# Kernel optimization log

Hardware: AMD Instinct MI355X
Metric: run time of the kernel (lower is better)

Reference implementation:

```python
import jax, jax.numpy as jnp
import numpy as np

M = 262144      # total tokens
K = 64          # n_channels (input dim)
N = 64          # expert_size (output dim)
E = 8           # n_experts


def setup_inputs() -> dict:
    key = jax.random.key(0)
    k1, k2, k3 = jax.random.split(key, 3)
    x = jax.random.normal(k1, (M, K), dtype=jnp.float32)
    sel = jax.random.randint(k2, (M,), 0, E, dtype=jnp.int32)
    w = jax.random.normal(k3, (E, K, N), dtype=jnp.float32)
    return {"x": x, "sel": sel, "w": w}


def reference(x, sel, w):
    # cvmm: out[m] = x[m] @ w[sel[m]]  (per-token expert GEMM)
    # Loop over the small fixed expert set; accumulate masked dense GEMMs
    # instead of materializing w[sel] ([M,K,N], which would be huge).
    E_ = w.shape[0]
    out = jnp.zeros((x.shape[0], w.shape[2]), dtype=x.dtype)
    for e in range(E_):
        mask = (sel == e)[:, None]           # [M,1]
        out = out + jnp.where(mask, x @ w[e], jnp.zeros((), x.dtype))
    return out
```

## Files before the change

kernel.cpp:

```cpp
#include <hip/hip_runtime.h>


typedef __bf16 bf16x8 __attribute__((ext_vector_type(8)));
typedef __bf16 bf16x4 __attribute__((ext_vector_type(4)));
typedef float  floatx4 __attribute__((ext_vector_type(4)));

#define CT 128

__global__ __launch_bounds__(256) void wpack_kernel(
    const float* __restrict__ w, bf16x8* __restrict__ wp)
{
    const int id   = blockIdx.x * 256 + threadIdx.x;
    const int lane = id & 63;
    const int nt   = (id >> 6) & 3;
    const int t    = (id >> 8) & 1;
    const int e    = id >> 9;
    const int q = lane >> 4, l16 = lane & 15;
    const float* src = w + (((e * 64) + t * 32 + q * 8) * 64) + nt * 16 + l16;
    bf16x8 f;
#pragma unroll
    for (int j = 0; j < 8; ++j) f[j] = (__bf16)src[j * 64];
    wp[id] = f;
}

__global__ __launch_bounds__(256, 3) void cvmm_kernel(
    const float* __restrict__ x,
    const int* __restrict__ sel,
    const bf16x8* __restrict__ wp,
    float* __restrict__ out)
{
    __shared__ __align__(16) unsigned char xls[CT * 128];
    __shared__ __align__(16) unsigned char obuf[CT * 272];
    __shared__ unsigned int sortLds[CT];
    __shared__ unsigned int invLds[CT];

    const int T    = threadIdx.x;
    const int lane = T & 63;
    const int wv   = T >> 6;
    const int q    = lane >> 4;
    const int l16  = lane & 15;

    const long tok0 = (long)blockIdx.x * CT;

    int s0 = 0, s1 = 0;
    if (wv == 0) {
        s0 = sel[tok0 + lane];
        s1 = sel[tok0 + 64 + lane];
    }

    const float* xb = x + tok0 * 64;
    floatx4 R[8];
#pragma unroll
    for (int i = 0; i < 8; ++i)
        R[i] = *(const floatx4*)(xb + i * 1024 + 4 * T);

    const bf16x8* wpw = wp + wv * 64 + lane;
    floatx4 bfp[8][2];
#pragma unroll
    for (int e = 0; e < 8; ++e) {
#pragma unroll
        for (int t = 0; t < 2; ++t)
            bfp[e][t] = __builtin_bit_cast(floatx4, wpw[e * 512 + t * 256]);
    }
#pragma unroll
    for (int e = 0; e < 8; ++e) {
        asm volatile("" : "+v"(bfp[e][0]), "+v"(bfp[e][1]));
    }

    if (wv == 0) {
        const unsigned long long lt = (1ull << lane) - 1;
        int slot0 = 0, slot1 = 0, pref = 0;
#pragma unroll
        for (int e = 0; e < 8; ++e) {
            unsigned long long m0 = __ballot(s0 == e);
            unsigned long long m1 = __ballot(s1 == e);
            if (s0 == e) slot0 = pref + __popcll(m0 & lt);
            if (s1 == e) slot1 = pref + __popcll(m0) + __popcll(m1 & lt);
            pref += __popcll(m0) + __popcll(m1);
        }
        invLds[lane]      = (unsigned)slot0;
        invLds[64 + lane] = (unsigned)slot1;
        sortLds[slot0] = (unsigned)lane        | ((unsigned)s0 << 8);
        sortLds[slot1] = (unsigned)(64 + lane) | ((unsigned)s1 << 8);
    }
    __syncthreads();

    {
        const int wrow = T >> 4;
        const int gl   = (T & 15) >> 1;
        const int half = (T & 1) * 8;
#pragma unroll
        for (int i = 0; i < 8; ++i) {
            const int slot = (int)invLds[i * 16 + wrow];
            bf16x4 v;
            v[0] = (__bf16)R[i][0]; v[1] = (__bf16)R[i][1];
            v[2] = (__bf16)R[i][2]; v[3] = (__bf16)R[i][3];
            *(bf16x4*)(xls + slot * 128 + ((gl ^ (slot & 7)) << 4) + half) = v;
        }
    }
    __syncthreads();

    {
        const int roffA = ((q)     ^ (l16 & 7)) << 4;
        const int roffB = ((q + 4) ^ (l16 & 7)) << 4;
        bf16x8 zf;
#pragma unroll
        for (int j = 0; j < 8; ++j) zf[j] = (__bf16)0.0f;

#pragma unroll
        for (int i = 0; i < 8; ++i) {
            const unsigned u = sortLds[i * 16 + l16];
            const int tokL = (int)(u & 255u);
            const int el   = (int)(u >> 8);
            const int rb   = (i * 16 + l16) * 128;
            const bf16x8 af0 = *(const bf16x8*)(xls + rb + roffA);
            const bf16x8 af1 = *(const bf16x8*)(xls + rb + roffB);
            const int elo = __builtin_amdgcn_readfirstlane(el);
            const int ehi = __builtin_amdgcn_readlane(el, 15);

            floatx4 acc = {0.0f, 0.0f, 0.0f, 0.0f};
#pragma unroll
            for (int e = 0; e < 8; ++e) {
                if (e >= elo && e <= ehi) {
                    const bool ok = (el == e);
                    acc = __builtin_amdgcn_mfma_f32_16x16x32_bf16(
                              __builtin_bit_cast(bf16x8, bfp[e][0]),
                              ok ? af0 : zf, acc, 0, 0, 0);
                    acc = __builtin_amdgcn_mfma_f32_16x16x32_bf16(
                              __builtin_bit_cast(bf16x8, bfp[e][1]),
                              ok ? af1 : zf, acc, 0, 0, 0);
                }
            }
            *(floatx4*)(obuf + tokL * 272 + (wv * 4 + q) * 16) = acc;
        }
    }
    __syncthreads();

    {
        float* og = out + tok0 * 64;
#pragma unroll
        for (int i = 0; i < 8; ++i) {
            const int G = i * 256 + T;
            const floatx4 v = *(const floatx4*)(obuf + (G >> 4) * 272 + (G & 15) * 16);
            *(floatx4*)(og + G * 4) = v;
        }
    }
}

extern "C" void kernel_launch(void* const* d_in, const int* in_sizes, int n_in,
                              void* d_out, int out_size, void* d_ws, size_t ws_size,
                              hipStream_t stream) {
    const float* x   = (const float*)d_in[0];
    const int*   sel = (const int*)d_in[1];
    const float* w   = (const float*)d_in[2];
    float*       out = (float*)d_out;

    const int M = in_sizes[0] / 64;
    bf16x8* wp = (bf16x8*)d_ws;

    wpack_kernel<<<16, 256, 0, stream>>>(w, wp);
    cvmm_kernel<<<M / CT, 256, 0, stream>>>(x, sel, wp, out);
}
```

Baseline: 121.4 us.

## Gather sorted x rows directly into LDS and fold weight packing into main kernel

Removes the separate weight-pack kernel: each block now loads and converts its fp32 weights to bf16 itself. The x tile is gathered in expert-sorted order straight into LDS as fp32 using global_load_lds, replacing the register staging and the inverse-permutation scatter. The output staging buffer reuses the x LDS region with an XOR swizzle, which frees LDS and raises the occupancy hint to 4 blocks per CU. The cost is redundant per-block weight reads and bf16 conversion, plus a larger fp32 x tile in LDS.

```diff
diff --git a/kernel.cpp b/kernel.cpp
--- a/kernel.cpp
+++ b/kernel.cpp
@@ -2,72 +2,43 @@
 
 
 typedef __bf16 bf16x8 __attribute__((ext_vector_type(8)));
-typedef __bf16 bf16x4 __attribute__((ext_vector_type(4)));
 typedef float  floatx4 __attribute__((ext_vector_type(4)));
 
 #define CT 128
 
-__global__ __launch_bounds__(256) void wpack_kernel(
-    const float* __restrict__ w, bf16x8* __restrict__ wp)
-{
-    const int id   = blockIdx.x * 256 + threadIdx.x;
-    const int lane = id & 63;
-    const int nt   = (id >> 6) & 3;
-    const int t    = (id >> 8) & 1;
-    const int e    = id >> 9;
-    const int q = lane >> 4, l16 = lane & 15;
-    const float* src = w + (((e * 64) + t * 32 + q * 8) * 64) + nt * 16 + l16;
-    bf16x8 f;
-#pragma unroll
-    for (int j = 0; j < 8; ++j) f[j] = (__bf16)src[j * 64];
-    wp[id] = f;
-}
+#define GLOAD_LDS16(g, l)                                        \
+    __builtin_amdgcn_global_load_lds(                            \
+        (const __attribute__((address_space(1))) void*)(g),      \
+        (__attribute__((address_space(3))) void*)(l), 16, 0, 0)
 
-__global__ __launch_bounds__(256, 3) void cvmm_kernel(
+#define BARL() do {                                        \
+    __builtin_amdgcn_sched_barrier(0);                     \
+    asm volatile("s_waitcnt lgkmcnt(0)" ::: "memory");     \
+    __builtin_amdgcn_s_barrier();                          \
+    __builtin_amdgcn_sched_barrier(0);                     \
+} while (0)
+
+__global__ __launch_bounds__(256, 4) void cvmm_kernel(
     const float* __restrict__ x,
     const int* __restrict__ sel,
-    const bf16x8* __restrict__ wp,
+    const float* __restrict__ w,
     float* __restrict__ out)
 {
-    __shared__ __align__(16) unsigned char xls[CT * 128];
-    __shared__ __align__(16) unsigned char obuf[CT * 272];
+    __shared__ __align__(16) unsigned char xls[CT * 256];
     __shared__ unsigned int sortLds[CT];
-    __shared__ unsigned int invLds[CT];
 
     const int T    = threadIdx.x;
     const int lane = T & 63;
     const int wv   = T >> 6;
     const int q    = lane >> 4;
     const int l16  = lane & 15;
+    const int n0   = wv << 4;
 
     const long tok0 = (long)blockIdx.x * CT;
 
-    int s0 = 0, s1 = 0;
     if (wv == 0) {
-        s0 = sel[tok0 + lane];
-        s1 = sel[tok0 + 64 + lane];
-    }
-
-    const float* xb = x + tok0 * 64;
-    floatx4 R[8];
-#pragma unroll
-    for (int i = 0; i < 8; ++i)
-        R[i] = *(const floatx4*)(xb + i * 1024 + 4 * T);
-
-    const bf16x8* wpw = wp + wv * 64 + lane;
-    floatx4 bfp[8][2];
-#pragma unroll
-    for (int e = 0; e < 8; ++e) {
-#pragma unroll
-        for (int t = 0; t < 2; ++t)
-            bfp[e][t] = __builtin_bit_cast(floatx4, wpw[e * 512 + t * 256]);
-    }
-#pragma unroll
-    for (int e = 0; e < 8; ++e) {
-        asm volatile("" : "+v"(bfp[e][0]), "+v"(bfp[e][1]));
-    }
-
-    if (wv == 0) {
+        const int s0 = sel[tok0 + lane];
+        const int s1 = sel[tok0 + 64 + lane];
         const unsigned long long lt = (1ull << lane) - 1;
         int slot0 = 0, slot1 = 0, pref = 0;
 #pragma unroll
@@ -78,71 +49,111 @@
             if (s1 == e) slot1 = pref + __popcll(m0) + __popcll(m1 & lt);
             pref += __popcll(m0) + __popcll(m1);
         }
-        invLds[lane]      = (unsigned)slot0;
-        invLds[64 + lane] = (unsigned)slot1;
         sortLds[slot0] = (unsigned)lane        | ((unsigned)s0 << 8);
         sortLds[slot1] = (unsigned)(64 + lane) | ((unsigned)s1 << 8);
     }
+
+    floatx4 bfp[8][2];
+#pragma unroll
+    for (int e = 0; e < 8; ++e)
+#pragma unroll
+        for (int t = 0; t < 2; ++t) {
+            const float* ws = w + ((e * 64 + t * 32 + q * 8) * 64) + (n0 + l16);
+            bf16x8 f;
+#pragma unroll
+            for (int j = 0; j < 8; ++j) f[j] = (__bf16)ws[j * 64];
+            bfp[e][t] = __builtin_bit_cast(floatx4, f);
+        }
+
+    BARL();
+
+    int tokA[8];
+#pragma unroll
+    for (int i = 0; i < 8; ++i) {
+        const int r    = i * 16 + wv * 4 + (lane >> 4);
+        const int tokR = (int)(sortLds[r] & 255u);
+        const int p    = (lane & 15) >> 1;
+        const int c    = p ^ (r & 7);
+        const float* g = x + (tok0 + tokR) * 64 + c * 8 + (lane & 1) * 4;
+        GLOAD_LDS16(g, xls + i * 4096 + wv * 1024);
+    }
+
+#pragma unroll
+    for (int i = 0; i < 8; ++i)
+        tokA[i] = (int)sortLds[i * 16 + l16];
+
+#pragma unroll
+    for (int e = 0; e < 8; ++e)
+        asm volatile("" : "+v"(bfp[e][0]), "+v"(bfp[e][1]));
+
     __syncthreads();
 
+    bf16x8 zf;
+#pragma unroll
+    for (int j = 0; j < 8; ++j) zf[j] = (__bf16)0.0f;
+
+    floatx4 acc[8];
+#pragma unroll
+    for (int i = 0; i < 8; ++i) {
+        const int el = tokA[i] >> 8;
+        const int r  = i * 16 + l16;
+        const int pA = (q)     ^ (r & 7);
+        const int pB = (q + 4) ^ (r & 7);
+        const float* fa = (const float*)(xls + r * 256 + pA * 32);
+        const float* fb = (const float*)(xls + r * 256 + pB * 32);
+        const floatx4 a0 = *(const floatx4*)(fa);
+        const floatx4 a1 = *(const floatx4*)(fa + 4);
+        const floatx4 b0 = *(const floatx4*)(fb);
+        const floatx4 b1 = *(const floatx4*)(fb + 4);
+        bf16x8 af0, af1;
+#pragma unroll
+        for (int j = 0; j < 4; ++j) {
+            af0[j] = (__bf16)a0[j]; af0[j + 4] = (__bf16)a1[j];
+            af1[j] = (__bf16)b0[j]; af1[j + 4] = (__bf16)b1[j];
+        }
+        const int elo = __builtin_amdgcn_readfirstlane(el);
+        const int ehi = __builtin_amdgcn_readlane(el, 15);
+
+        floatx4 a = {0.0f, 0.0f, 0.0f, 0.0f};
+#pragma unroll
+        for (int e = 0; e < 8; ++e) {
+            if (e >= elo && e <= ehi) {
+                const bool ok = (el == e);
+                a = __builtin_amdgcn_mfma_f32_16x16x32_bf16(
+                        __builtin_bit_cast(bf16x8, bfp[e][0]),
+                        ok ? af0 : zf, a, 0, 0, 0);
+                a = __builtin_amdgcn_mfma_f32_16x16x32_bf16(
+                        __builtin_bit_cast(bf16x8, bfp[e][1]),
+                        ok ? af1 : zf, a, 0, 0, 0);
+            }
+        }
+        acc[i] = a;
+    }
+
+    BARL();
+
     {
-        const int wrow = T >> 4;
-        const int gl   = (T & 15) >> 1;
-        const int half = (T & 1) * 8;
+        const int g  = wv * 4 + q;
+        const int gh = (g & 1) * 16;
+        const int gc = g >> 1;
 #pragma unroll
         for (int i = 0; i < 8; ++i) {
-            const int slot = (int)invLds[i * 16 + wrow];
-            bf16x4 v;
-            v[0] = (__bf16)R[i][0]; v[1] = (__bf16)R[i][1];
-            v[2] = (__bf16)R[i][2]; v[3] = (__bf16)R[i][3];
-            *(bf16x4*)(xls + slot * 128 + ((gl ^ (slot & 7)) << 4) + half) = v;
+            const int tokL = tokA[i] & 255;
+            *(floatx4*)(xls + tokL * 256 + ((gc ^ (tokL & 7)) << 5) + gh) = acc[i];
         }
     }
-    __syncthreads();
 
-    {
-        const int roffA = ((q)     ^ (l16 & 7)) << 4;
-        const int roffB = ((q + 4) ^ (l16 & 7)) << 4;
-        bf16x8 zf;
-#pragma unroll
-        for (int j = 0; j < 8; ++j) zf[j] = (__bf16)0.0f;
-
-#pragma unroll
-        for (int i = 0; i < 8; ++i) {
-            const unsigned u = sortLds[i * 16 + l16];
-            const int tokL = (int)(u & 255u);
-            const int el   = (int)(u >> 8);
-            const int rb   = (i * 16 + l16) * 128;
-            const bf16x8 af0 = *(const bf16x8*)(xls + rb + roffA);
-            const bf16x8 af1 = *(const bf16x8*)(xls + rb + roffB);
-            const int elo = __builtin_amdgcn_readfirstlane(el);
-            const int ehi = __builtin_amdgcn_readlane(el, 15);
-
-            floatx4 acc = {0.0f, 0.0f, 0.0f, 0.0f};
-#pragma unroll
-            for (int e = 0; e < 8; ++e) {
-                if (e >= elo && e <= ehi) {
-                    const bool ok = (el == e);
-                    acc = __builtin_amdgcn_mfma_f32_16x16x32_bf16(
-                              __builtin_bit_cast(bf16x8, bfp[e][0]),
-                              ok ? af0 : zf, acc, 0, 0, 0);
-                    acc = __builtin_amdgcn_mfma_f32_16x16x32_bf16(
-                              __builtin_bit_cast(bf16x8, bfp[e][1]),
-                              ok ? af1 : zf, acc, 0, 0, 0);
-                }
-            }
-            *(floatx4*)(obuf + tokL * 272 + (wv * 4 + q) * 16) = acc;
-        }
-    }
-    __syncthreads();
+    BARL();
 
     {
         float* og = out + tok0 * 64;
 #pragma unroll
         for (int i = 0; i < 8; ++i) {
             const int G = i * 256 + T;
-            const floatx4 v = *(const floatx4*)(obuf + (G >> 4) * 272 + (G & 15) * 16);
-            *(floatx4*)(og + G * 4) = v;
+            const int r = G >> 4, g = G & 15;
+            const floatx4 v = *(const floatx4*)(
+                xls + r * 256 + ((((g >> 1) ^ (r & 7))) << 5) + (g & 1) * 16);
+            *(floatx4*)(og + (long)G * 4) = v;
         }
     }
 }
@@ -156,8 +167,5 @@
     float*       out = (float*)d_out;
 
     const int M = in_sizes[0] / 64;
-    bf16x8* wp = (bf16x8*)d_ws;
-
-    wpack_kernel<<<16, 256, 0, stream>>>(w, wp);
-    cvmm_kernel<<<M / CT, 256, 0, stream>>>(x, sel, wp, out);
+    cvmm_kernel<<<M / CT, 256, 0, stream>>>(x, sel, w, out);
 }
```

After: 127.5 us. 5.0% more time.
